# Performance work log

Hardware: AMD Instinct MI355X
Metric: run time of the kernel (lower is better)

Reference implementation:

```python
import jax, jax.numpy as jnp
import numpy as np

# dims: B=batch, S=seq len, H=heads, D=in_features per head, R=realizations, K=conv kernel
B, S, H, D, R, K = 2, 1024, 8, 64, 32, 128


def setup_inputs() -> dict:
    key = jax.random.key(0)
    kq, kk, kwq, kwk, kz = jax.random.split(key, 5)
    queries = jax.random.normal(kq, (B, S, H, D), jnp.float32)
    keys = jax.random.normal(kk, (B, S, H, D), jnp.float32)
    # depthwise conv weights, torch init: uniform[0,1), shape (C_out, 1, K) with groups=C_out
    wq = jax.random.uniform(kwq, (H * D, 1, K), jnp.float32)
    wk = jax.random.uniform(kwk, (H * D, 1, K), jnp.float32)
    # stochastic process noise z: (B*R, H*D, 4K+S), scaled by 1/sqrt(R*D)
    z = jax.random.normal(kz, (B * R, H * D, 4 * K + S), jnp.float32) / np.float32(np.sqrt(R * D))
    return {"queries": queries, "keys": keys, "wq": wq, "wk": wk, "z": z}


def _dwconv(x, w):
    # depthwise 1D cross-correlation, VALID padding (matches nn.Conv1d, groups=C)
    return jax.lax.conv_general_dilated(
        x, w, window_strides=(1,), padding='VALID',
        dimension_numbers=('NCH', 'OIH', 'NCH'),
        feature_group_count=w.shape[0])


def reference(queries, keys, wq, wk, z):
    # note the faithful swap from the source: kbar uses conv_q, qbar uses conv_k
    kbar = _dwconv(z, wq)[:, :, K:K + S].reshape(B, R, H, D, S)
    qbar = _dwconv(z, wk)[:, :, K:K + S].reshape(B, R, H, D, S)
    # fused broadcast-multiply + feature-dim reduction:
    # (qbar * queries[:,None]).sum(axis=3) then permute -> (B,S,H,R)
    qhat = jnp.einsum('brhds,bshd->bshr', qbar, queries)
    khat = jnp.einsum('brhds,bshd->bshr', kbar, keys)
    return qhat, khat
```

## Files before the change

kernel.cpp:

```cpp
#include <hip/hip_runtime.h>

#define BB 2
#define SS 1024
#define HH 8
#define DD 64
#define RR 32
#define KK 128
#define ZLEN 1536
#define HD 512

#define MS 256
#define DC 16
#define NTC 24
#define WROWS 192
#define WSEG (WROWS*DC)
#define PARTS_FLOATS (256*8*2*64*16)

typedef _Float16 f16x8 __attribute__((ext_vector_type(8)));
typedef _Float16 f16x2 __attribute__((ext_vector_type(2)));
typedef float    f32x16 __attribute__((ext_vector_type(16)));

__global__ __launch_bounds__(512) void convspe_mfma(
    const float* __restrict__ q, const float* __restrict__ kmat,
    const float* __restrict__ wq, const float* __restrict__ wk,
    const float* __restrict__ z, float* __restrict__ parts)
{
    __shared__ __align__(16) _Float16 zbuf[2][16 * 32 * 16];
    __shared__ __align__(16) _Float16 wqs[WSEG];
    __shared__ __align__(16) _Float16 wks[WSEG];

    const int tid  = threadIdx.x;
    const int wave = __builtin_amdgcn_readfirstlane(tid >> 6);
    const int lane = tid & 63;
    const int rl   = lane & 31;
    const int hi   = lane >> 5;

    const int bx = blockIdx.x;
    const int dc = bx & 3, stile = (bx >> 2) & 3, h = (bx >> 4) & 7, b = bx >> 7;
    const int s0b = stile * MS;
    const int d0  = dc * DC;

    const int sr  = tid >> 4;
    const int sth = (tid >> 3) & 1;
    const int sdp = tid & 7;
    const float* zr0 = z + ((size_t)(b * RR + sr) * HD + h * DD + d0 + 2 * sdp) * ZLEN
                         + KK + s0b + sth * 8;
    const float* zr1 = zr0 + ZLEN;

    float4 ra[2], rb[2];
    auto loadchunk = [&](int tc) {
        const float4* p0 = (const float4*)(zr0 + tc * 16);
        const float4* p1 = (const float4*)(zr1 + tc * 16);
        #pragma unroll
        for (int i = 0; i < 2; ++i) { ra[i] = p0[i]; rb[i] = p1[i]; }
    };
    auto writechunk = [&](int p) {
        f16x2* dst = (f16x2*)zbuf[p];
        #pragma unroll
        for (int i = 0; i < 2; ++i) {
            const float av[4] = {ra[i].x, ra[i].y, ra[i].z, ra[i].w};
            const float bv[4] = {rb[i].x, rb[i].y, rb[i].z, rb[i].w};
            #pragma unroll
            for (int e = 0; e < 4; ++e) {
                const int ts = sth * 8 + i * 4 + e;
                dst[(ts * 32 + sr) * 8 + sdp] =
                    __builtin_bit_cast(f16x2, __builtin_amdgcn_cvt_pkrtz(av[e], bv[e]));
            }
        }
    };

    loadchunk(0);

    f16x8 qf, kf;
    {
        const int s = s0b + wave * 32 + rl;
        const size_t base = (((size_t)b * SS + s) * HH + h) * DD + d0 + 8 * hi;
        #pragma unroll
        for (int j = 0; j < 8; ++j) {
            qf[j] = (_Float16)q[base + j];
            kf[j] = (_Float16)kmat[base + j];
        }
    }

    {
        const int di = tid & 15, tq = tid >> 4;
        const int grow = (h * DD + dc * DC + di) * KK + tq * 4;
        const float4 vq4 = *(const float4*)&wq[grow];
        const float4 vk4 = *(const float4*)&wk[grow];
        const float aq[4] = {vq4.x, vq4.y, vq4.z, vq4.w};
        const float ak[4] = {vk4.x, vk4.y, vk4.z, vk4.w};
        #pragma unroll
        for (int e = 0; e < 4; ++e) {
            const int ds = (tq * 4 + e + 32) * 16 + di;
            wqs[ds] = (_Float16)aq[e];
            wks[ds] = (_Float16)ak[e];
        }
        wqs[tid] = (_Float16)0.f;        wks[tid] = (_Float16)0.f;
        wqs[2560 + tid] = (_Float16)0.f; wks[2560 + tid] = (_Float16)0.f;
    }

    f32x16 accq, acck;
    #pragma unroll
    for (int j = 0; j < 16; ++j) { accq[j] = 0.f; acck[j] = 0.f; }

    writechunk(0);
    loadchunk(1);
    __syncthreads();

    for (int tc = 0; tc < NTC; ++tc) {
        const int p = tc & 1;
        const int tqbase = tc * 16 - wave * 32;
        const int lo  = (tqbase < 0) ? -tqbase : 0;
        const int hi_ = (160 - tqbase < 16) ? (160 - tqbase) : 16;
        if (lo < hi_) {
            const _Float16* zb = zbuf[p];
            auto zrd = [&](int ts) {
                return *(const f16x8*)&zb[(ts * 32 + rl) * 16 + 8 * hi];
            };
            auto wrd = [&](const _Float16* ws, int ts) {
                const int row = tqbase + ts - rl + 32;
                return *(const f16x8*)&ws[row * 16 + 8 * hi];
            };
            f16x8 a0 = zrd(lo), k0 = wrd(wks, lo), q0 = wrd(wqs, lo);
            f16x8 a1 = a0, k1 = k0, q1 = q0;
            if (lo + 1 < hi_) { a1 = zrd(lo + 1); k1 = wrd(wks, lo + 1); q1 = wrd(wqs, lo + 1); }
            for (int ts = lo; ts < hi_ - 2; ++ts) {
                const f16x8 a2 = zrd(ts + 2), k2 = wrd(wks, ts + 2), q2 = wrd(wqs, ts + 2);
                accq = __builtin_amdgcn_mfma_f32_32x32x16_f16(a0, k0 * qf, accq, 0, 0, 0);
                acck = __builtin_amdgcn_mfma_f32_32x32x16_f16(a0, q0 * kf, acck, 0, 0, 0);
                a0 = a1; k0 = k1; q0 = q1;
                a1 = a2; k1 = k2; q1 = q2;
            }
            accq = __builtin_amdgcn_mfma_f32_32x32x16_f16(a0, k0 * qf, accq, 0, 0, 0);
            acck = __builtin_amdgcn_mfma_f32_32x32x16_f16(a0, q0 * kf, acck, 0, 0, 0);
            if (lo + 1 < hi_) {
                accq = __builtin_amdgcn_mfma_f32_32x32x16_f16(a1, k1 * qf, accq, 0, 0, 0);
                acck = __builtin_amdgcn_mfma_f32_32x32x16_f16(a1, q1 * kf, acck, 0, 0, 0);
            }
        }
        if (tc + 1 < NTC) writechunk((tc + 1) & 1);
        if (tc + 2 < NTC) loadchunk(tc + 2);
        __syncthreads();
    }

    {
        float* pq = parts + ((((size_t)bx * 8 + wave) * 2 + 0) * 64 + lane) * 16;
        float* pk = parts + ((((size_t)bx * 8 + wave) * 2 + 1) * 64 + lane) * 16;
        #pragma unroll
        for (int g = 0; g < 4; ++g) {
            *(float4*)&pq[g * 4] = make_float4(accq[4*g], accq[4*g+1], accq[4*g+2], accq[4*g+3]);
            *(float4*)&pk[g * 4] = make_float4(acck[4*g], acck[4*g+1], acck[4*g+2], acck[4*g+3]);
        }
    }
}

__global__ __launch_bounds__(256) void reduce_kernel(
    const float* __restrict__ parts, float* __restrict__ out)
{
    const int idx = blockIdx.x * 256 + threadIdx.x;
    const int rq = idx & 7, h = (idx >> 3) & 7, s = (idx >> 6) & 1023;
    const int b = (idx >> 16) & 1, o = idx >> 17;
    const int stile = s >> 8, sub = (s >> 5) & 7, rl = s & 31;

    const int off = ((rq & 1) * 32 + rl) * 16 + 4 * (rq >> 1);

    float4 acc = make_float4(0.f, 0.f, 0.f, 0.f);
    #pragma unroll
    for (int dc = 0; dc < 4; ++dc) {
        const int bx = ((b * 8 + h) * 4 + stile) * 4 + dc;
        const float4 v = *(const float4*)&parts[(((size_t)bx * 8 + sub) * 2 + o) * 1024 + off];
        acc.x += v.x; acc.y += v.y; acc.z += v.z; acc.w += v.w;
    }
    *(float4*)&out[(size_t)idx * 4] = acc;
}

extern "C" void kernel_launch(void* const* d_in, const int* in_sizes, int n_in,
                              void* d_out, int out_size, void* d_ws, size_t ws_size,
                              hipStream_t stream) {
    const float* q  = (const float*)d_in[0];
    const float* k  = (const float*)d_in[1];
    const float* wq = (const float*)d_in[2];
    const float* wk = (const float*)d_in[3];
    const float* z  = (const float*)d_in[4];
    float* out = (float*)d_out;

    float* parts = (float*)d_ws;

    hipLaunchKernelGGL(convspe_mfma, dim3(256), dim3(512), 0, stream,
                       q, k, wq, wk, z, parts);
    hipLaunchKernelGGL(reduce_kernel, dim3(1024), dim3(256), 0, stream, parts, out);
}
```

Baseline: 306.6 us.

## Double block to 1024 threads, split K-loop across wave halves with LDS merge

Each block now runs 16 waves instead of 8. Two waves share each 32-row output tile, one taking the even tap steps and the other the odd ones, and their accumulators are merged through shared memory at the end. Global z loads and weight staging are spread across twice as many threads, so each thread issues fewer loads. The goal is more latency hiding and MFMA issue parallelism with only 256 blocks, at the cost of extra barriers, an LDS reduction, and a 1024-thread launch bound that may cap registers per thread.

```diff
diff --git a/kernel.cpp b/kernel.cpp
--- a/kernel.cpp
+++ b/kernel.cpp
@@ -20,7 +20,7 @@
 typedef _Float16 f16x2 __attribute__((ext_vector_type(2)));
 typedef float    f32x16 __attribute__((ext_vector_type(16)));
 
-__global__ __launch_bounds__(512) void convspe_mfma(
+__global__ __launch_bounds__(1024) void convspe_mfma(
     const float* __restrict__ q, const float* __restrict__ kmat,
     const float* __restrict__ wq, const float* __restrict__ wk,
     const float* __restrict__ z, float* __restrict__ parts)
@@ -30,7 +30,9 @@
     __shared__ __align__(16) _Float16 wks[WSEG];
 
     const int tid  = threadIdx.x;
-    const int wave = __builtin_amdgcn_readfirstlane(tid >> 6);
+    const int wv   = tid >> 6;
+    const int ssub = __builtin_amdgcn_readfirstlane(wv & 7);
+    const int half = __builtin_amdgcn_readfirstlane(wv >> 3);
     const int lane = tid & 63;
     const int rl   = lane & 31;
     const int hi   = lane >> 5;
@@ -40,32 +42,27 @@
     const int s0b = stile * MS;
     const int d0  = dc * DC;
 
-    const int sr  = tid >> 4;
-    const int sth = (tid >> 3) & 1;
-    const int sdp = tid & 7;
+    const int sr  = tid >> 5;
+    const int sdp = (tid >> 2) & 7;
+    const int sth = tid & 3;
     const float* zr0 = z + ((size_t)(b * RR + sr) * HD + h * DD + d0 + 2 * sdp) * ZLEN
-                         + KK + s0b + sth * 8;
+                         + KK + s0b + sth * 4;
     const float* zr1 = zr0 + ZLEN;
 
-    float4 ra[2], rb[2];
+    float4 ra, rb;
     auto loadchunk = [&](int tc) {
-        const float4* p0 = (const float4*)(zr0 + tc * 16);
-        const float4* p1 = (const float4*)(zr1 + tc * 16);
-        #pragma unroll
-        for (int i = 0; i < 2; ++i) { ra[i] = p0[i]; rb[i] = p1[i]; }
+        ra = *(const float4*)(zr0 + tc * 16);
+        rb = *(const float4*)(zr1 + tc * 16);
     };
     auto writechunk = [&](int p) {
         f16x2* dst = (f16x2*)zbuf[p];
-        #pragma unroll
-        for (int i = 0; i < 2; ++i) {
-            const float av[4] = {ra[i].x, ra[i].y, ra[i].z, ra[i].w};
-            const float bv[4] = {rb[i].x, rb[i].y, rb[i].z, rb[i].w};
-            #pragma unroll
-            for (int e = 0; e < 4; ++e) {
-                const int ts = sth * 8 + i * 4 + e;
-                dst[(ts * 32 + sr) * 8 + sdp] =
-                    __builtin_bit_cast(f16x2, __builtin_amdgcn_cvt_pkrtz(av[e], bv[e]));
-            }
+        const float av[4] = {ra.x, ra.y, ra.z, ra.w};
+        const float bv[4] = {rb.x, rb.y, rb.z, rb.w};
+        #pragma unroll
+        for (int e = 0; e < 4; ++e) {
+            const int ts = sth * 4 + e;
+            dst[(ts * 32 + sr) * 8 + sdp] =
+                __builtin_bit_cast(f16x2, __builtin_amdgcn_cvt_pkrtz(av[e], bv[e]));
         }
     };
 
@@ -73,7 +70,7 @@
 
     f16x8 qf, kf;
     {
-        const int s = s0b + wave * 32 + rl;
+        const int s = s0b + ssub * 32 + rl;
         const size_t base = (((size_t)b * SS + s) * HH + h) * DD + d0 + 8 * hi;
         #pragma unroll
         for (int j = 0; j < 8; ++j) {
@@ -83,20 +80,17 @@
     }
 
     {
-        const int di = tid & 15, tq = tid >> 4;
-        const int grow = (h * DD + dc * DC + di) * KK + tq * 4;
-        const float4 vq4 = *(const float4*)&wq[grow];
-        const float4 vk4 = *(const float4*)&wk[grow];
-        const float aq[4] = {vq4.x, vq4.y, vq4.z, vq4.w};
-        const float ak[4] = {vk4.x, vk4.y, vk4.z, vk4.w};
-        #pragma unroll
-        for (int e = 0; e < 4; ++e) {
-            const int ds = (tq * 4 + e + 32) * 16 + di;
-            wqs[ds] = (_Float16)aq[e];
-            wks[ds] = (_Float16)ak[e];
-        }
-        wqs[tid] = (_Float16)0.f;        wks[tid] = (_Float16)0.f;
-        wqs[2560 + tid] = (_Float16)0.f; wks[2560 + tid] = (_Float16)0.f;
+        const int t2 = tid & 511;
+        const int di = t2 & 15, tq = t2 >> 4;
+        const float* warr = (tid < 512) ? wq : wk;
+        _Float16* wdst    = (tid < 512) ? wqs : wks;
+        const float4 v4 = *(const float4*)&warr[(h * DD + dc * DC + di) * KK + tq * 4];
+        const float av[4] = {v4.x, v4.y, v4.z, v4.w};
+        #pragma unroll
+        for (int e = 0; e < 4; ++e)
+            wdst[(tq * 4 + e + 32) * 16 + di] = (_Float16)av[e];
+        wdst[t2] = (_Float16)0.f;
+        wdst[2560 + t2] = (_Float16)0.f;
     }
 
     f32x16 accq, acck;
@@ -109,10 +103,11 @@
 
     for (int tc = 0; tc < NTC; ++tc) {
         const int p = tc & 1;
-        const int tqbase = tc * 16 - wave * 32;
+        const int tqbase = tc * 16 - ssub * 32;
         const int lo  = (tqbase < 0) ? -tqbase : 0;
         const int hi_ = (160 - tqbase < 16) ? (160 - tqbase) : 16;
-        if (lo < hi_) {
+        const int ps  = lo + ((lo ^ half) & 1);
+        if (ps < hi_) {
             const _Float16* zb = zbuf[p];
             auto zrd = [&](int ts) {
                 return *(const f16x8*)&zb[(ts * 32 + rl) * 16 + 8 * hi];
@@ -121,11 +116,11 @@
                 const int row = tqbase + ts - rl + 32;
                 return *(const f16x8*)&ws[row * 16 + 8 * hi];
             };
-            f16x8 a0 = zrd(lo), k0 = wrd(wks, lo), q0 = wrd(wqs, lo);
+            f16x8 a0 = zrd(ps), k0 = wrd(wks, ps), q0 = wrd(wqs, ps);
             f16x8 a1 = a0, k1 = k0, q1 = q0;
-            if (lo + 1 < hi_) { a1 = zrd(lo + 1); k1 = wrd(wks, lo + 1); q1 = wrd(wqs, lo + 1); }
-            for (int ts = lo; ts < hi_ - 2; ++ts) {
-                const f16x8 a2 = zrd(ts + 2), k2 = wrd(wks, ts + 2), q2 = wrd(wqs, ts + 2);
+            if (ps + 2 < hi_) { a1 = zrd(ps + 2); k1 = wrd(wks, ps + 2); q1 = wrd(wqs, ps + 2); }
+            for (int ts = ps; ts < hi_ - 4; ts += 2) {
+                const f16x8 a2 = zrd(ts + 4), k2 = wrd(wks, ts + 4), q2 = wrd(wqs, ts + 4);
                 accq = __builtin_amdgcn_mfma_f32_32x32x16_f16(a0, k0 * qf, accq, 0, 0, 0);
                 acck = __builtin_amdgcn_mfma_f32_32x32x16_f16(a0, q0 * kf, acck, 0, 0, 0);
                 a0 = a1; k0 = k1; q0 = q1;
@@ -133,7 +128,7 @@
             }
             accq = __builtin_amdgcn_mfma_f32_32x32x16_f16(a0, k0 * qf, accq, 0, 0, 0);
             acck = __builtin_amdgcn_mfma_f32_32x32x16_f16(a0, q0 * kf, acck, 0, 0, 0);
-            if (lo + 1 < hi_) {
+            if (ps + 2 < hi_) {
                 accq = __builtin_amdgcn_mfma_f32_32x32x16_f16(a1, k1 * qf, accq, 0, 0, 0);
                 acck = __builtin_amdgcn_mfma_f32_32x32x16_f16(a1, q1 * kf, acck, 0, 0, 0);
             }
@@ -144,8 +139,32 @@
     }
 
     {
-        float* pq = parts + ((((size_t)bx * 8 + wave) * 2 + 0) * 64 + lane) * 16;
-        float* pk = parts + ((((size_t)bx * 8 + wave) * 2 + 1) * 64 + lane) * 16;
+        float* mrg = (float*)zbuf;
+        const int col = ssub * 64 + lane;
+        if (half == 1) {
+            #pragma unroll
+            for (int j = 0; j < 16; ++j) mrg[j * 512 + col] = accq[j];
+        }
+        __syncthreads();
+        if (half == 0) {
+            #pragma unroll
+            for (int j = 0; j < 16; ++j) accq[j] += mrg[j * 512 + col];
+        }
+        __syncthreads();
+        if (half == 1) {
+            #pragma unroll
+            for (int j = 0; j < 16; ++j) mrg[j * 512 + col] = acck[j];
+        }
+        __syncthreads();
+        if (half == 0) {
+            #pragma unroll
+            for (int j = 0; j < 16; ++j) acck[j] += mrg[j * 512 + col];
+        }
+    }
+
+    if (half == 0) {
+        float* pq = parts + ((((size_t)bx * 8 + ssub) * 2 + 0) * 64 + lane) * 16;
+        float* pk = parts + ((((size_t)bx * 8 + ssub) * 2 + 1) * 64 + lane) * 16;
         #pragma unroll
         for (int g = 0; g < 4; ++g) {
             *(float4*)&pq[g * 4] = make_float4(accq[4*g], accq[4*g+1], accq[4*g+2], accq[4*g+3]);
@@ -186,7 +205,7 @@
 
     float* parts = (float*)d_ws;
 
-    hipLaunchKernelGGL(convspe_mfma, dim3(256), dim3(512), 0, stream,
+    hipLaunchKernelGGL(convspe_mfma, dim3(256), dim3(1024), 0, stream,
                        q, k, wq, wk, z, parts);
     hipLaunchKernelGGL(reduce_kernel, dim3(1024), dim3(256), 0, stream, parts, out);
 }
```

Result: faster. 300.2 us (-2.1%).
